# Kernel tuning notes

Hardware: AMD Instinct MI355X
Metric: run time of the kernel (lower is better)

Reference implementation:

```python
import jax, jax.numpy as jnp
import numpy as np

N_USER, N_ITEM, D = 50000, 100000, 64
E_UI, E_UU = 1000000, 800000
NEG_SLOPE = 0.2


def gatv2(x_src, x_dst, src_idx, dst_idx, w_src, w_dst, attn, bias, n_dst):
    """DGL GATv2Conv, num_heads=1: e = a . leaky_relu(Ws x_u + Wd x_v),
    segment-softmax over edges incoming to each dst node, message = Ws x_u."""
    hs = x_src @ w_src                      # [Ns, D]
    hd = x_dst @ w_dst                      # [Nd, D]
    pre = jax.nn.leaky_relu(hs[src_idx] + hd[dst_idx], NEG_SLOPE)  # [E, D]
    e = pre @ attn                          # [E]
    emax = jax.ops.segment_max(e, dst_idx, num_segments=n_dst)     # -inf for empty
    a = jnp.exp(e - emax[dst_idx])          # [E]
    denom = jax.ops.segment_sum(a, dst_idx, num_segments=n_dst)    # [Nd]
    num = jax.ops.segment_sum(hs[src_idx] * a[:, None], dst_idx, num_segments=n_dst)
    out = num / jnp.maximum(denom, 1e-9)[:, None]
    return out + bias


def setup_inputs() -> dict:
    key = jax.random.key(0)
    ks = jax.random.split(key, 32)
    s = 1.0 / np.sqrt(D)
    def W(k):
        return jax.random.normal(k, (D, D), jnp.float32) * s
    inp = {
        "h_user": jax.random.normal(ks[0], (N_USER, D), jnp.float32),
        "h_item": jax.random.normal(ks[1], (N_ITEM, D), jnp.float32),
        "rate_src": jax.random.randint(ks[2], (E_UI,), 0, N_USER, jnp.int32),
        "rate_dst": jax.random.randint(ks[3], (E_UI,), 0, N_ITEM, jnp.int32),
        "rb_src": jax.random.randint(ks[4], (E_UI,), 0, N_ITEM, jnp.int32),
        "rb_dst": jax.random.randint(ks[5], (E_UI,), 0, N_USER, jnp.int32),
        "link_src": jax.random.randint(ks[6], (E_UU,), 0, N_USER, jnp.int32),
        "link_dst": jax.random.randint(ks[7], (E_UU,), 0, N_USER, jnp.int32),
    }
    names = ["r1", "rb1", "rb2", "l2"]
    for i, nm in enumerate(names):
        inp[f"w_src_{nm}"] = W(ks[8 + 4 * i])
        inp[f"w_dst_{nm}"] = W(ks[9 + 4 * i])
        inp[f"a_{nm}"] = jax.random.normal(ks[10 + 4 * i], (D,), jnp.float32) * s
        inp[f"b_{nm}"] = jnp.zeros((D,), jnp.float32)
    inp["w_out"] = jax.random.normal(ks[24], (2 * D, D), jnp.float32) * (1.0 / np.sqrt(2 * D))
    inp["b_out"] = jnp.zeros((D,), jnp.float32)
    return inp


def reference(h_user, h_item,
              w_src_r1, w_dst_r1, a_r1, b_r1,
              w_src_rb1, w_dst_rb1, a_rb1, b_rb1,
              w_src_rb2, w_dst_rb2, a_rb2, b_rb2,
              w_src_l2, w_dst_l2, a_l2, b_l2,
              w_out, b_out,
              rate_src, rate_dst, rb_src, rb_dst, link_src, link_dst):
    # layer1 'rate': user -> item
    h1_item = gatv2(h_user, h_item, rate_src, rate_dst,
                    w_src_r1, w_dst_r1, a_r1, b_r1, N_ITEM)
    # layer1 'rated-by': item -> user
    h2_user = gatv2(h_item, h_user, rb_src, rb_dst,
                    w_src_rb1, w_dst_rb1, a_rb1, b_rb1, N_USER)
    # layer2 'rated-by': item(h1) -> user
    infl_user = gatv2(h1_item, h_user, rb_src, rb_dst,
                      w_src_rb2, w_dst_rb2, a_rb2, b_rb2, N_USER)
    # layer2 'link': user(h2) -> user
    social_user = gatv2(h2_user, h_user, link_src, link_dst,
                        w_src_l2, w_dst_l2, a_l2, b_l2, N_USER)
    out = jnp.concatenate([infl_user, social_user], axis=1) @ w_out + b_out
    return out
```

## Files before the change

kernel.cpp:

```cpp
#include <hip/hip_runtime.h>
#include <hip/hip_fp16.h>
#include <math.h>

#define N_USER 50000
#define N_ITEM 100000
#define E_UI   1000000
#define E_UU   800000
#define E_TOT  (E_UI + E_UI + E_UU)
#define NEG_SLOPE 0.2f
#define LOG2E 1.4426950408889634f

#define NB0 391
#define NB1 196
#define NB2 196
#define NBTOT (NB0 + NB1 + NB2)
#define GPB 256
#define MATN (NBTOT * 256)
#define NBP  ((MATN + 1023) / 1024)

#define XS_STRIDE 68

typedef _Float16 h2v __attribute__((ext_vector_type(2)));

#if defined(__has_builtin)
#if __has_builtin(__builtin_amdgcn_fdot2)
#define HAS_FDOT2 1
#endif
#if __has_builtin(__builtin_elementwise_max)
#define HAS_EW_MAX 1
#endif
#if __has_builtin(__builtin_amdgcn_exp2f)
#define HAS_EXP2 1
#endif
#endif

__device__ __forceinline__ float fexp2(float x) {
#ifdef HAS_EXP2
  return __builtin_amdgcn_exp2f(x);
#else
  return exp2f(x);
#endif
}

__device__ __forceinline__ float fdot2acc(__half2 a, __half2 b, float c) {
#ifdef HAS_FDOT2
  return __builtin_amdgcn_fdot2(__builtin_bit_cast(h2v, a), __builtin_bit_cast(h2v, b), c, false);
#else
  float2 af = __half22float2(a), bf = __half22float2(b);
  return fmaf(af.x, bf.x, fmaf(af.y, bf.y, c));
#endif
}

__device__ __forceinline__ __half2 h2max(__half2 a, __half2 b) {
  h2v av = __builtin_bit_cast(h2v, a), bv = __builtin_bit_cast(h2v, b);
#ifdef HAS_EW_MAX
  h2v r = __builtin_elementwise_max(av, bv);
#else
  h2v r; r.x = av.x > bv.x ? av.x : bv.x; r.y = av.y > bv.y ? av.y : bv.y;
#endif
  return __builtin_bit_cast(__half2, r);
}

__device__ __forceinline__ __half2 h2min(__half2 a, __half2 b) {
  h2v av = __builtin_bit_cast(h2v, a), bv = __builtin_bit_cast(h2v, b);
#ifdef HAS_EW_MAX
  h2v r = __builtin_elementwise_min(av, bv);
#else
  h2v r; r.x = av.x < bv.x ? av.x : bv.x; r.y = av.y < bv.y ? av.y : bv.y;
#endif
  return __builtin_bit_cast(__half2, r);
}


__global__ __launch_bounds__(256) void bucket_hist(const int* __restrict__ d0, const int* __restrict__ d1,
                                                   const int* __restrict__ d2, int* __restrict__ mat) {
  int gid = blockIdx.x >> 8;
  int g   = blockIdx.x & 255;
  const int* dst = gid == 0 ? d0 : (gid == 1 ? d1 : d2);
  int E    = (gid == 2) ? E_UU : E_UI;
  int NB   = (gid == 0) ? NB0 : NB1;
  int boff = (gid == 0) ? 0 : (gid == 1 ? NB0 : NB0 + NB1);
  __shared__ int cnt[NB0];
  for (int b = threadIdx.x; b < NB; b += 256) cnt[b] = 0;
  __syncthreads();
  int chunk = (E + 255) >> 8;
  int lo = g * chunk, hi = min(lo + chunk, E);
  for (int i = lo + threadIdx.x; i < hi; i += 256)
    atomicAdd(&cnt[dst[i] >> 8], 1);
  __syncthreads();
  for (int b = threadIdx.x; b < NB; b += 256)
    mat[(boff + b) * 256 + g] = cnt[b];
}


__global__ __launch_bounds__(256) void partial_kernel(const int* __restrict__ counts, int n,
                                                      int* __restrict__ partials) {
  int t = threadIdx.x;
  int base = blockIdx.x * 1024 + t * 4;
  int s = 0;
  if (base + 3 < n) {
    int4 v = *(const int4*)(counts + base);
    s = v.x + v.y + v.z + v.w;
  } else {
    for (int i = base; i < n && i < base + 4; ++i) s += counts[i];
  }
  #pragma unroll
  for (int off = 1; off < 64; off <<= 1) s += __shfl_xor(s, off);
  __shared__ int ws[4];
  if ((t & 63) == 0) ws[t >> 6] = s;
  __syncthreads();
  if (t == 0) partials[blockIdx.x] = ws[0] + ws[1] + ws[2] + ws[3];
}

__global__ __launch_bounds__(256) void scan_apply_fused(const int* __restrict__ counts, int n,
                                                        const int* __restrict__ partials, int nbp,
                                                        int* __restrict__ outp) {
  __shared__ int sp[256];
  int t = threadIdx.x;
  sp[t] = (t < nbp) ? partials[t] : 0;
  __syncthreads();
  for (int off = 1; off < 256; off <<= 1) {
    int v = (t >= off) ? sp[t - off] : 0;
    __syncthreads();
    sp[t] += v;
    __syncthreads();
  }
  int block_off = (blockIdx.x == 0) ? 0 : sp[blockIdx.x - 1];

  int base = blockIdx.x * 1024 + t * 4;
  int4 v = make_int4(0, 0, 0, 0);
  if (base + 3 < n) {
    v = *(const int4*)(counts + base);
  } else {
    int* pv = &v.x;
    for (int i = 0; i < 4; ++i) if (base + i < n) pv[i] = counts[base + i];
  }
  int s = v.x + v.y + v.z + v.w;
  int lane = t & 63;
  int wv = t >> 6;
  int inc = s;
  #pragma unroll
  for (int off = 1; off < 64; off <<= 1) {
    int u = __shfl_up(inc, off);
    if (lane >= off) inc += u;
  }
  __shared__ int wsum[4];
  if (lane == 63) wsum[wv] = inc;
  __syncthreads();
  int woff = 0;
  for (int i = 0; i < wv; ++i) woff += wsum[i];
  int excl = woff + (inc - s) + block_off;
  int4 rp;
  rp.x = excl;
  rp.y = rp.x + v.x;
  rp.z = rp.y + v.y;
  rp.w = rp.z + v.z;
  if (base + 3 < n) {
    *(int4*)(outp + base) = rp;
  } else {
    int* pr = &rp.x;
    for (int i = 0; i < 4; ++i) if (base + i < n) outp[base + i] = pr[i];
  }
}


__global__ __launch_bounds__(256) void bucket_scatter(const int* __restrict__ s0v, const int* __restrict__ d0,
                                                      const int* __restrict__ s1v, const int* __restrict__ d1,
                                                      const int* __restrict__ s2v, const int* __restrict__ d2,
                                                      const int* __restrict__ mscan, unsigned int* __restrict__ pairs) {
  int gid = blockIdx.x >> 8;
  int g   = blockIdx.x & 255;
  const int* src = gid == 0 ? s0v : (gid == 1 ? s1v : s2v);
  const int* dst = gid == 0 ? d0  : (gid == 1 ? d1  : d2);
  int E    = (gid == 2) ? E_UU : E_UI;
  int NB   = (gid == 0) ? NB0 : NB1;
  int boff = (gid == 0) ? 0 : (gid == 1 ? NB0 : NB0 + NB1);
  __shared__ int cur[NB0];
  for (int b = threadIdx.x; b < NB; b += 256) cur[b] = mscan[(boff + b) * 256 + g];
  __syncthreads();
  int chunk = (E + 255) >> 8;
  int lo = g * chunk, hi = min(lo + chunk, E);
  for (int i = lo + threadIdx.x; i < hi; i += 256) {
    int d = dst[i], s = src[i];
    int pos = atomicAdd(&cur[d >> 8], 1);
    pairs[pos] = ((unsigned)(d & 255) << 24) | (unsigned)s;
  }
}


__global__ __launch_bounds__(256) void bucket_finalize(const unsigned int* __restrict__ pairs,
                                                       const int* __restrict__ mscan,
                                                       int* __restrict__ rp, int* __restrict__ col) {
  int gb = blockIdx.x;
  int t  = threadIdx.x;
  int gid  = (gb < NB0) ? 0 : (gb < NB0 + NB1 ? 1 : 2);
  int boff = (gid == 0) ? 0 : (gid == 1 ? NB0 : NB0 + NB1);
  int node_goff = (gid == 0) ? 0 : (gid == 1 ? N_ITEM : N_ITEM + N_USER);
  int n    = (gid == 0) ? N_ITEM : N_USER;
  int b_local = gb - boff;
  int bs = mscan[gb * 256];
  int be = (gb + 1 < NBTOT) ? mscan[(gb + 1) * 256] : E_TOT;

  __shared__ int cnt[256];
  __shared__ int curb[256];
  __shared__ int wsum[4];
  cnt[t] = 0;
  __syncthreads();
  for (int i = bs + t; i < be; i += 256)
    atomicAdd(&cnt[pairs[i] >> 24], 1);
  __syncthreads();

  int v = cnt[t];
  int lane = t & 63, wv = t >> 6;
  int inc = v;
  #pragma unroll
  for (int off = 1; off < 64; off <<= 1) {
    int u = __shfl_up(inc, off);
    if (lane >= off) inc += u;
  }
  if (lane == 63) wsum[wv] = inc;
  __syncthreads();
  int woff = 0;
  for (int i = 0; i < wv; ++i) woff += wsum[i];
  int base = bs + woff + (inc - v);

  int node_local = b_local * 256 + t;
  if (node_local < n) rp[node_goff + node_local] = base;
  if (gb == NBTOT - 1 && t == 255) rp[N_ITEM + 2 * N_USER] = E_TOT;
  curb[t] = base;
  __syncthreads();

  for (int i = bs + t; i < be; i += 256) {
    unsigned u = pairs[i];
    int p = atomicAdd(&curb[u >> 24], 1);
    col[p] = (int)(u & 0xFFFFFFu);
  }
}


__device__ __forceinline__ void load_xtile(const float* __restrict__ X, float* Xs, int base, int N) {
  #pragma unroll
  for (int i = 0; i < 4; ++i) {
    int idx = threadIdx.x * 4 + i * 1024;
    int row = idx >> 6, colc = idx & 63;
    int grow = base + row;
    const float* src = X + (size_t)(grow < N ? grow : N - 1) * 64 + colc;
    *(float4*)(Xs + row * XS_STRIDE + colc) = *(const float4*)src;
  }
}

__device__ __forceinline__ void gemm_phase(const float* __restrict__ Wsrc, float* Ws,
                                           const float* x0, const float* x1,
                                           const float* x2, const float* x3, int c4,
                                           float4& acc0, float4& acc1, float4& acc2, float4& acc3) {
  __syncthreads();
  #pragma unroll
  for (int i = 0; i < 4; ++i) {
    int idx = threadIdx.x * 4 + i * 1024;
    *(float4*)(Ws + idx) = *(const float4*)(Wsrc + idx);
  }
  __syncthreads();
  acc0 = make_float4(0.f, 0.f, 0.f, 0.f);
  acc1 = acc0; acc2 = acc0; acc3 = acc0;
  #pragma unroll 4
  for (int k4 = 0; k4 < 64; k4 += 4) {
    float4 xa = *(const float4*)(x0 + k4);
    float4 xb = *(const float4*)(x1 + k4);
    float4 xc = *(const float4*)(x2 + k4);
    float4 xd = *(const float4*)(x3 + k4);
    #pragma unroll
    for (int kk = 0; kk < 4; ++kk) {
      float4 w = *(const float4*)(Ws + (k4 + kk) * 64 + c4);
      float sa = (&xa.x)[kk], sb = (&xb.x)[kk], sc = (&xc.x)[kk], sd = (&xd.x)[kk];
      acc0.x = fmaf(sa, w.x, acc0.x); acc0.y = fmaf(sa, w.y, acc0.y);
      acc0.z = fmaf(sa, w.z, acc0.z); acc0.w = fmaf(sa, w.w, acc0.w);
      acc1.x = fmaf(sb, w.x, acc1.x); acc1.y = fmaf(sb, w.y, acc1.y);
      acc1.z = fmaf(sb, w.z, acc1.z); acc1.w = fmaf(sb, w.w, acc1.w);
      acc2.x = fmaf(sc, w.x, acc2.x); acc2.y = fmaf(sc, w.y, acc2.y);
      acc2.z = fmaf(sc, w.z, acc2.z); acc2.w = fmaf(sc, w.w, acc2.w);
      acc3.x = fmaf(sd, w.x, acc3.x); acc3.y = fmaf(sd, w.y, acc3.y);
      acc3.z = fmaf(sd, w.z, acc3.z); acc3.w = fmaf(sd, w.w, acc3.w);
    }
  }
}

__device__ __forceinline__ void gemm_phase_h(const float* __restrict__ Wsrc, float* Ws,
                                             const __half* x0, const __half* x1,
                                             const __half* x2, const __half* x3, int c4,
                                             float4& acc0, float4& acc1, float4& acc2, float4& acc3) {
  __syncthreads();
  #pragma unroll
  for (int i = 0; i < 4; ++i) {
    int idx = threadIdx.x * 4 + i * 1024;
    *(float4*)(Ws + idx) = *(const float4*)(Wsrc + idx);
  }
  __syncthreads();
  acc0 = make_float4(0.f, 0.f, 0.f, 0.f);
  acc1 = acc0; acc2 = acc0; acc3 = acc0;
  #pragma unroll 4
  for (int k4 = 0; k4 < 64; k4 += 4) {
    uint2 ua = *(const uint2*)(x0 + k4);
    uint2 ub = *(const uint2*)(x1 + k4);
    uint2 uc = *(const uint2*)(x2 + k4);
    uint2 ud = *(const uint2*)(x3 + k4);
    float2 fa0 = __half22float2(__builtin_bit_cast(__half2, ua.x));
    float2 fa1 = __half22float2(__builtin_bit_cast(__half2, ua.y));
    float2 fb0 = __half22float2(__builtin_bit_cast(__half2, ub.x));
    float2 fb1 = __half22float2(__builtin_bit_cast(__half2, ub.y));
    float2 fc0 = __half22float2(__builtin_bit_cast(__half2, uc.x));
    float2 fc1 = __half22float2(__builtin_bit_cast(__half2, uc.y));
    float2 fd0 = __half22float2(__builtin_bit_cast(__half2, ud.x));
    float2 fd1 = __half22float2(__builtin_bit_cast(__half2, ud.y));
    float xav[4] = {fa0.x, fa0.y, fa1.x, fa1.y};
    float xbv[4] = {fb0.x, fb0.y, fb1.x, fb1.y};
    float xcv[4] = {fc0.x, fc0.y, fc1.x, fc1.y};
    float xdv[4] = {fd0.x, fd0.y, fd1.x, fd1.y};
    #pragma unroll
    for (int kk = 0; kk < 4; ++kk) {
      float4 w = *(const float4*)(Ws + (k4 + kk) * 64 + c4);
      float sa = xav[kk], sb = xbv[kk], sc = xcv[kk], sd = xdv[kk];
      acc0.x = fmaf(sa, w.x, acc0.x); acc0.y = fmaf(sa, w.y, acc0.y);
      acc0.z = fmaf(sa, w.z, acc0.z); acc0.w = fmaf(sa, w.w, acc0.w);
      acc1.x = fmaf(sb, w.x, acc1.x); acc1.y = fmaf(sb, w.y, acc1.y);
      acc1.z = fmaf(sb, w.z, acc1.z); acc1.w = fmaf(sb, w.w, acc1.w);
      acc2.x = fmaf(sc, w.x, acc2.x); acc2.y = fmaf(sc, w.y, acc2.y);
      acc2.z = fmaf(sc, w.z, acc2.z); acc2.w = fmaf(sc, w.w, acc2.w);
      acc3.x = fmaf(sd, w.x, acc3.x); acc3.y = fmaf(sd, w.y, acc3.y);
      acc3.z = fmaf(sd, w.z, acc3.z); acc3.w = fmaf(sd, w.w, acc3.w);
    }
  }
}

__device__ __forceinline__ void store4_f16(__half* __restrict__ Y, int r0, int r1, int r2, int r3,
                                           int N, int c4,
                                           const float4& a0, const float4& a1,
                                           const float4& a2, const float4& a3) {
  uint2 st;
  if (r0 < N) {
    st.x = __builtin_bit_cast(unsigned int, __floats2half2_rn(a0.x, a0.y));
    st.y = __builtin_bit_cast(unsigned int, __floats2half2_rn(a0.z, a0.w));
    *(uint2*)(Y + (size_t)r0 * 64 + c4) = st;
  }
  if (r1 < N) {
    st.x = __builtin_bit_cast(unsigned int, __floats2half2_rn(a1.x, a1.y));
    st.y = __builtin_bit_cast(unsigned int, __floats2half2_rn(a1.z, a1.w));
    *(uint2*)(Y + (size_t)r1 * 64 + c4) = st;
  }
  if (r2 < N) {
    st.x = __builtin_bit_cast(unsigned int, __floats2half2_rn(a2.x, a2.y));
    st.y = __builtin_bit_cast(unsigned int, __floats2half2_rn(a2.z, a2.w));
    *(uint2*)(Y + (size_t)r2 * 64 + c4) = st;
  }
  if (r3 < N) {
    st.x = __builtin_bit_cast(unsigned int, __floats2half2_rn(a3.x, a3.y));
    st.y = __builtin_bit_cast(unsigned int, __floats2half2_rn(a3.z, a3.w));
    *(uint2*)(Y + (size_t)r3 * 64 + c4) = st;
  }
}

__global__ __launch_bounds__(256) void gemm_user4(const float* __restrict__ X,
                                                  const float* __restrict__ W0, const float* __restrict__ W1,
                                                  const float* __restrict__ W2, const float* __restrict__ W3,
                                                  __half* __restrict__ Y0, __half* __restrict__ Y1,
                                                  __half* __restrict__ Y2, __half* __restrict__ Y3, int N) {
  __shared__ float Xs[64 * XS_STRIDE];
  __shared__ float Ws[64 * 64];
  int base = blockIdx.x * 64;
  load_xtile(X, Xs, base, N);
  int c4 = (threadIdx.x & 15) * 4;
  int rl = threadIdx.x >> 4;
  int r0 = base + rl, r1 = r0 + 16, r2 = r0 + 32, r3 = r0 + 48;
  const float* x0 = Xs + (rl +  0) * XS_STRIDE;
  const float* x1 = Xs + (rl + 16) * XS_STRIDE;
  const float* x2 = Xs + (rl + 32) * XS_STRIDE;
  const float* x3 = Xs + (rl + 48) * XS_STRIDE;
  float4 a0, a1, a2, a3;
  gemm_phase(W0, Ws, x0, x1, x2, x3, c4, a0, a1, a2, a3);
  store4_f16(Y0, r0, r1, r2, r3, N, c4, a0, a1, a2, a3);
  gemm_phase(W1, Ws, x0, x1, x2, x3, c4, a0, a1, a2, a3);
  store4_f16(Y1, r0, r1, r2, r3, N, c4, a0, a1, a2, a3);
  gemm_phase(W2, Ws, x0, x1, x2, x3, c4, a0, a1, a2, a3);
  store4_f16(Y2, r0, r1, r2, r3, N, c4, a0, a1, a2, a3);
  gemm_phase(W3, Ws, x0, x1, x2, x3, c4, a0, a1, a2, a3);
  store4_f16(Y3, r0, r1, r2, r3, N, c4, a0, a1, a2, a3);
}

__global__ __launch_bounds__(256) void gemm_item2(const float* __restrict__ X,
                                                  const float* __restrict__ W0, const float* __restrict__ W1,
                                                  __half* __restrict__ Y0, __half* __restrict__ Y1, int N) {
  __shared__ float Xs[64 * XS_STRIDE];
  __shared__ float Ws[64 * 64];
  int base = blockIdx.x * 64;
  load_xtile(X, Xs, base, N);
  int c4 = (threadIdx.x & 15) * 4;
  int rl = threadIdx.x >> 4;
  int r0 = base + rl, r1 = r0 + 16, r2 = r0 + 32, r3 = r0 + 48;
  const float* x0 = Xs + (rl +  0) * XS_STRIDE;
  const float* x1 = Xs + (rl + 16) * XS_STRIDE;
  const float* x2 = Xs + (rl + 32) * XS_STRIDE;
  const float* x3 = Xs + (rl + 48) * XS_STRIDE;
  float4 a0, a1, a2, a3;
  gemm_phase(W0, Ws, x0, x1, x2, x3, c4, a0, a1, a2, a3);
  store4_f16(Y0, r0, r1, r2, r3, N, c4, a0, a1, a2, a3);
  gemm_phase(W1, Ws, x0, x1, x2, x3, c4, a0, a1, a2, a3);
  store4_f16(Y1, r0, r1, r2, r3, N, c4, a0, a1, a2, a3);
}

__global__ __launch_bounds__(256) void gemm_mid2x(const __half* __restrict__ XA, const float* __restrict__ WA,
                                                  __half* __restrict__ YA, int NA, int nbA,
                                                  const __half* __restrict__ XB, const float* __restrict__ WB,
                                                  __half* __restrict__ YB, int NB_) {
  __shared__ float Ws[64 * 64];
  const __half* X; const float* W; __half* Y; int N; int base;
  if ((int)blockIdx.x < nbA) {
    X = XA; W = WA; Y = YA; N = NA; base = blockIdx.x * 64;
  } else {
    X = XB; W = WB; Y = YB; N = NB_; base = (blockIdx.x - nbA) * 64;
  }
  int c4 = (threadIdx.x & 15) * 4;
  int rl = threadIdx.x >> 4;
  int r0 = base + rl, r1 = r0 + 16, r2 = r0 + 32, r3 = r0 + 48;
  const __half* x0 = X + (size_t)(r0 < N ? r0 : N - 1) * 64;
  const __half* x1 = X + (size_t)(r1 < N ? r1 : N - 1) * 64;
  const __half* x2 = X + (size_t)(r2 < N ? r2 : N - 1) * 64;
  const __half* x3 = X + (size_t)(r3 < N ? r3 : N - 1) * 64;
  float4 a0, a1, a2, a3;
  gemm_phase_h(W, Ws, x0, x1, x2, x3, c4, a0, a1, a2, a3);
  store4_f16(Y, r0, r1, r2, r3, N, c4, a0, a1, a2, a3);
}


__global__ __launch_bounds__(256) void gat8n_kernel(
    const __half* __restrict__ hsA, const __half* __restrict__ hdAp,
    const int* __restrict__ rpA, const float* __restrict__ attnA, const float* __restrict__ biasA,
    __half* __restrict__ outA, int NdA,
    const __half* __restrict__ hsB, const __half* __restrict__ hdBp,
    const int* __restrict__ rpB, const float* __restrict__ attnB, const float* __restrict__ biasB,
    __half* __restrict__ outB, int NdB,
    const int* __restrict__ col) {
  int w = (blockIdx.x * blockDim.x + threadIdx.x) >> 6;
  int grp = (threadIdx.x >> 3) & 7;
  int q   = threadIdx.x & 7;
  int node = w * 8 + grp;
  bool valid = node < NdA + NdB;
  bool inA = node < NdA;
  const __half* hs  = inA ? hsA  : hsB;
  const __half* hd  = inA ? hdAp : hdBp;
  const int* rp     = inA ? rpA  : rpB;
  const float* attn = inA ? attnA : attnB;
  const float* bias = inA ? biasA : biasB;
  __half* outp      = inA ? outA : outB;
  int nn = inA ? node : node - NdA;
  if (!valid) nn = 0;
  int s0 = valid ? rp[nn] : 0;
  int s1 = valid ? rp[nn + 1] : 0;

  const __half2 C02 = __floats2half2_rn(NEG_SLOPE, NEG_SLOPE);
  const __half2 Z   = __floats2half2_rn(0.f, 0.f);

  __half2 hd2[4], a2[4];
  {
    uint4 hv = *(const uint4*)(hd + (size_t)nn * 64 + q * 8);
    hd2[0] = __builtin_bit_cast(__half2, hv.x);
    hd2[1] = __builtin_bit_cast(__half2, hv.y);
    hd2[2] = __builtin_bit_cast(__half2, hv.z);
    hd2[3] = __builtin_bit_cast(__half2, hv.w);
    const float* ap = attn + q * 8;
    #pragma unroll
    for (int i = 0; i < 2; ++i) {
      float4 v = *(const float4*)(ap + i * 4);
      a2[2 * i]     = __floats2half2_rn(v.x * LOG2E, v.y * LOG2E);
      a2[2 * i + 1] = __floats2half2_rn(v.z * LOG2E, v.w * LOG2E);
    }
  }

  float m = -1e30f, den = 0.f;
  float num[8];
  #pragma unroll
  for (int i = 0; i < 8; ++i) num[i] = 0.f;

  for (int e = s0; e < s1; e += 4) {
    bool h1 = (e + 1) < s1, h2c = (e + 2) < s1, h3 = (e + 3) < s1;
    int sa = col[e];
    int sb = col[h1 ? e + 1 : e];
    int sc = col[h2c ? e + 2 : e];
    int sd = col[h3 ? e + 3 : e];
    uint4 ra = *(const uint4*)(hs + (size_t)sa * 64 + q * 8);
    uint4 rb = *(const uint4*)(hs + (size_t)sb * 64 + q * 8);
    uint4 rc = *(const uint4*)(hs + (size_t)sc * 64 + q * 8);
    uint4 rd = *(const uint4*)(hs + (size_t)sd * 64 + q * 8);
    unsigned rau[4] = {ra.x, ra.y, ra.z, ra.w};
    unsigned rbu[4] = {rb.x, rb.y, rb.z, rb.w};
    unsigned rcu[4] = {rc.x, rc.y, rc.z, rc.w};
    unsigned rdu[4] = {rd.x, rd.y, rd.z, rd.w};

    float ta = 0.f, tb = 0.f, tc = 0.f, td = 0.f;
    #pragma unroll
    for (int i = 0; i < 4; ++i) {
      __half2 xa = __hadd2(__builtin_bit_cast(__half2, rau[i]), hd2[i]);
      ta = fdot2acc(a2[i], __hfma2(C02, h2min(xa, Z), h2max(xa, Z)), ta);
      __half2 xb = __hadd2(__builtin_bit_cast(__half2, rbu[i]), hd2[i]);
      tb = fdot2acc(a2[i], __hfma2(C02, h2min(xb, Z), h2max(xb, Z)), tb);
      __half2 xc = __hadd2(__builtin_bit_cast(__half2, rcu[i]), hd2[i]);
      tc = fdot2acc(a2[i], __hfma2(C02, h2min(xc, Z), h2max(xc, Z)), tc);
      __half2 xd = __hadd2(__builtin_bit_cast(__half2, rdu[i]), hd2[i]);
      td = fdot2acc(a2[i], __hfma2(C02, h2min(xd, Z), h2max(xd, Z)), td);
    }
    #pragma unroll
    for (int off = 1; off < 8; off <<= 1) {
      ta += __shfl_xor(ta, off);
      tb += __shfl_xor(tb, off);
      tc += __shfl_xor(tc, off);
      td += __shfl_xor(td, off);
    }
    if (!h1)  tb = -1e30f;
    if (!h2c) tc = -1e30f;
    if (!h3)  td = -1e30f;

    float tp = fmaxf(fmaxf(ta, tb), fmaxf(tc, td));
    float dd = tp - m;
    if (dd > 11.5f) {
      float sc0 = fexp2(-dd);
      den *= sc0;
      #pragma unroll
      for (int i = 0; i < 8; ++i) num[i] *= sc0;
      m = tp;
    }
    float pa = fexp2(ta - m);
    float pb = fexp2(tb - m);
    float pc = fexp2(tc - m);
    float pd = fexp2(td - m);
    den += (pa + pb) + (pc + pd);
    __half2 pab = __floats2half2_rn(pa, pb);
    __half2 pcd = __floats2half2_rn(pc, pd);

    #pragma unroll
    for (int i = 0; i < 4; ++i) {
      unsigned lo_ab = (rau[i] & 0xFFFFu) | (rbu[i] << 16);
      unsigned hi_ab = (rau[i] >> 16) | (rbu[i] & 0xFFFF0000u);
      unsigned lo_cd = (rcu[i] & 0xFFFFu) | (rdu[i] << 16);
      unsigned hi_cd = (rcu[i] >> 16) | (rdu[i] & 0xFFFF0000u);
      num[2 * i]     = fdot2acc(__builtin_bit_cast(__half2, lo_cd), pcd,
                       fdot2acc(__builtin_bit_cast(__half2, lo_ab), pab, num[2 * i]));
      num[2 * i + 1] = fdot2acc(__builtin_bit_cast(__half2, hi_cd), pcd,
                       fdot2acc(__builtin_bit_cast(__half2, hi_ab), pab, num[2 * i + 1]));
    }
  }

  if (valid) {
    float inv = 1.f / fmaxf(den, 1e-9f);
    const float* bp = bias + q * 8;
    float4 b0 = *(const float4*)(bp);
    float4 b1 = *(const float4*)(bp + 4);
    uint4 st;
    st.x = __builtin_bit_cast(unsigned int,
        __floats2half2_rn(fmaf(num[0], inv, b0.x), fmaf(num[1], inv, b0.y)));
    st.y = __builtin_bit_cast(unsigned int,
        __floats2half2_rn(fmaf(num[2], inv, b0.z), fmaf(num[3], inv, b0.w)));
    st.z = __builtin_bit_cast(unsigned int,
        __floats2half2_rn(fmaf(num[4], inv, b1.x), fmaf(num[5], inv, b1.y)));
    st.w = __builtin_bit_cast(unsigned int,
        __floats2half2_rn(fmaf(num[6], inv, b1.z), fmaf(num[7], inv, b1.w)));
    *(uint4*)(outp + (size_t)nn * 64 + q * 8) = st;
  }
}


__global__ __launch_bounds__(256) void final_kernel(const __half* __restrict__ A, const __half* __restrict__ B,
                                                    const float* __restrict__ W, const float* __restrict__ bias,
                                                    float* __restrict__ Y, int N) {
  __shared__ float Ws[128 * 64];
  #pragma unroll
  for (int i = 0; i < 8; ++i) {
    int idx = threadIdx.x * 4 + i * 1024;
    *(float4*)(Ws + idx) = *(const float4*)(W + idx);
  }
  __syncthreads();
  int c4 = (threadIdx.x & 15) * 4;
  int rl = threadIdx.x >> 4;
  int base = blockIdx.x * 64;

  float4 b4 = *(const float4*)(bias + c4);

  #pragma unroll
  for (int rr = 0; rr < 4; ++rr) {
    int row = base + rr * 16 + rl;
    if (row >= N) continue;
    const __half* ar = A + (size_t)row * 64;
    const __half* br = B + (size_t)row * 64;
    float4 acc = b4;
    #pragma unroll 4
    for (int k4 = 0; k4 < 64; k4 += 4) {
      uint2 ua = *(const uint2*)(ar + k4);
      uint2 ub = *(const uint2*)(br + k4);
      float2 fa0 = __half22float2(__builtin_bit_cast(__half2, ua.x));
      float2 fa1 = __half22float2(__builtin_bit_cast(__half2, ua.y));
      float2 fb0 = __half22float2(__builtin_bit_cast(__half2, ub.x));
      float2 fb1 = __half22float2(__builtin_bit_cast(__half2, ub.y));
      float xav[4] = {fa0.x, fa0.y, fa1.x, fa1.y};
      float xbv[4] = {fb0.x, fb0.y, fb1.x, fb1.y};
      #pragma unroll
      for (int kk = 0; kk < 4; ++kk) {
        float4 wa = *(const float4*)(Ws + (k4 + kk) * 64 + c4);
        float4 wb = *(const float4*)(Ws + (64 + k4 + kk) * 64 + c4);
        float xsa = xav[kk], xsb = xbv[kk];
        acc.x = fmaf(xsa, wa.x, acc.x); acc.x = fmaf(xsb, wb.x, acc.x);
        acc.y = fmaf(xsa, wa.y, acc.y); acc.y = fmaf(xsb, wb.y, acc.y);
        acc.z = fmaf(xsa, wa.z, acc.z); acc.z = fmaf(xsb, wb.z, acc.z);
        acc.w = fmaf(xsa, wa.w, acc.w); acc.w = fmaf(xsb, wb.w, acc.w);
      }
    }
    *(float4*)(Y + (size_t)row * 64 + c4) = acc;
  }
}


extern "C" void kernel_launch(void* const* d_in, const int* in_sizes, int n_in,
                              void* d_out, int out_size, void* d_ws, size_t ws_size,
                              hipStream_t stream) {
  const float* h_user   = (const float*)d_in[0];
  const float* h_item   = (const float*)d_in[1];
  const int* rate_src   = (const int*)d_in[2];
  const int* rate_dst   = (const int*)d_in[3];
  const int* rb_src     = (const int*)d_in[4];
  const int* rb_dst     = (const int*)d_in[5];
  const int* link_src   = (const int*)d_in[6];
  const int* link_dst   = (const int*)d_in[7];
  const float* w_src_r1  = (const float*)d_in[8];
  const float* w_dst_r1  = (const float*)d_in[9];
  const float* a_r1      = (const float*)d_in[10];
  const float* b_r1      = (const float*)d_in[11];
  const float* w_src_rb1 = (const float*)d_in[12];
  const float* w_dst_rb1 = (const float*)d_in[13];
  const float* a_rb1     = (const float*)d_in[14];
  const float* b_rb1     = (const float*)d_in[15];
  const float* w_src_rb2 = (const float*)d_in[16];
  const float* w_dst_rb2 = (const float*)d_in[17];
  const float* a_rb2     = (const float*)d_in[18];
  const float* b_rb2     = (const float*)d_in[19];
  const float* w_src_l2  = (const float*)d_in[20];
  const float* w_dst_l2  = (const float*)d_in[21];
  const float* a_l2      = (const float*)d_in[22];
  const float* b_l2      = (const float*)d_in[23];
  const float* w_out     = (const float*)d_in[24];
  const float* b_out     = (const float*)d_in[25];
  float* out = (float*)d_out;

  char* ws = (char*)d_ws;
  size_t off = 0;
  auto alloc = [&](size_t bytes) -> void* {
    void* p = ws + off;
    off += (bytes + 255) & ~(size_t)255;
    return p;
  };

  __half* uh0 = (__half*)alloc((size_t)N_USER * 64 * 2);
  __half* u1  = (__half*)alloc((size_t)N_USER * 64 * 2);
  __half* u2  = (__half*)alloc((size_t)N_USER * 64 * 2);
  __half* u3  = (__half*)alloc((size_t)N_USER * 64 * 2);
  __half* i0  = (__half*)alloc((size_t)N_ITEM * 64 * 2);
  __half* ih1 = (__half*)alloc((size_t)N_ITEM * 64 * 2);

  int* mat     = (int*)alloc((size_t)MATN * 4);
  int* mscan   = (int*)alloc((size_t)MATN * 4);
  int* partials= (int*)alloc(256 * 4);
  int* grp     = (int*)alloc((size_t)(N_ITEM + 2 * N_USER + 1) * 4);
  unsigned int* pairs = (unsigned int*)alloc((size_t)E_TOT * 4);
  int* col_all = (int*)alloc((size_t)E_TOT * 4);

  bucket_hist<<<3 * GPB, 256, 0, stream>>>(rate_dst, rb_dst, link_dst, mat);
  partial_kernel<<<NBP, 256, 0, stream>>>(mat, MATN, partials);
  scan_apply_fused<<<NBP, 256, 0, stream>>>(mat, MATN, partials, NBP, mscan);
  bucket_scatter<<<3 * GPB, 256, 0, stream>>>(rate_src, rate_dst, rb_src, rb_dst,
                                              link_src, link_dst, mscan, pairs);
  bucket_finalize<<<NBTOT, 256, 0, stream>>>(pairs, mscan, grp, col_all);

  int* rp_rate = grp;
  int* rp_rb   = grp + N_ITEM;
  int* rp_link = grp + N_ITEM + N_USER;

  gemm_user4<<<(N_USER + 63) / 64, 256, 0, stream>>>(
      h_user, w_src_r1, w_dst_rb1, w_dst_rb2, w_dst_l2, uh0, u1, u2, u3, N_USER);
  gemm_item2<<<(N_ITEM + 63) / 64, 256, 0, stream>>>(
      h_item, w_dst_r1, w_src_rb1, i0, ih1, N_ITEM);

  {
    int nodes = N_ITEM + N_USER;
    gat8n_kernel<<<(nodes + 31) / 32, 256, 0, stream>>>(
        uh0, i0, rp_rate, a_r1,  b_r1,  i0, N_ITEM,
        ih1, u1, rp_rb,   a_rb1, b_rb1, u1, N_USER,
        col_all);
  }

  {
    int nbA = (N_ITEM + 63) / 64;
    int nbB = (N_USER + 63) / 64;
    gemm_mid2x<<<nbA + nbB, 256, 0, stream>>>(
        i0, w_src_rb2, ih1, N_ITEM, nbA,
        u1, w_src_l2,  uh0, N_USER);
  }

  {
    int nodes = N_USER + N_USER;
    gat8n_kernel<<<(nodes + 31) / 32, 256, 0, stream>>>(
        ih1, u2, rp_rb,   a_rb2, b_rb2, u2, N_USER,
        uh0, u3, rp_link, a_l2,  b_l2,  u3, N_USER,
        col_all);
  }

  final_kernel<<<(N_USER + 63) / 64, 256, 0, stream>>>(u2, u3, w_out, b_out, out, N_USER);
}
```

Before: 258.3 us.

## Sort destination nodes by in-degree to balance GAT aggregation warps

Builds a per-region degree histogram in bucket_finalize, scans it, and scatters node ids into a degree-sorted permutation. The GAT kernels then process nodes through that permutation, so the 8 nodes sharing a wavefront have similar edge counts and divergence from uneven degrees is reduced. This adds two small kernels, a memset and global atomics on a 192-bin histogram, and it breaks the locality of hd and output accesses, which now follow permuted node order.

Result: slower. 933.0 us (+261.2%).

```diff
diff --git a/kernel.cpp b/kernel.cpp
--- a/kernel.cpp
+++ b/kernel.cpp
@@ -7,6 +7,7 @@
 #define E_UI   1000000
 #define E_UU   800000
 #define E_TOT  (E_UI + E_UI + E_UU)
+#define NTOT_NODES (N_ITEM + 2 * N_USER)
 #define NEG_SLOPE 0.2f
 #define LOG2E 1.4426950408889634f
 
@@ -190,7 +191,8 @@
 
 __global__ __launch_bounds__(256) void bucket_finalize(const unsigned int* __restrict__ pairs,
                                                        const int* __restrict__ mscan,
-                                                       int* __restrict__ rp, int* __restrict__ col) {
+                                                       int* __restrict__ rp, int* __restrict__ col,
+                                                       int* __restrict__ degbins) {
   int gb = blockIdx.x;
   int t  = threadIdx.x;
   int gid  = (gb < NB0) ? 0 : (gb < NB0 + NB1 ? 1 : 2);
@@ -225,7 +227,10 @@
   int base = bs + woff + (inc - v);
 
   int node_local = b_local * 256 + t;
-  if (node_local < n) rp[node_goff + node_local] = base;
+  if (node_local < n) {
+    rp[node_goff + node_local] = base;
+    atomicAdd(&degbins[gid * 64 + (v < 63 ? v : 63)], 1);
+  }
   if (gb == NBTOT - 1 && t == 255) rp[N_ITEM + 2 * N_USER] = E_TOT;
   curb[t] = base;
   __syncthreads();
@@ -235,6 +240,27 @@
     int p = atomicAdd(&curb[u >> 24], 1);
     col[p] = (int)(u & 0xFFFFFFu);
   }
+}
+
+
+__global__ void bin_scan(const int* __restrict__ bins, int* __restrict__ cursor) {
+  int r = threadIdx.x;
+  if (r < 3) {
+    int acc = 0;
+    for (int b = 0; b < 64; ++b) { cursor[r * 64 + b] = acc; acc += bins[r * 64 + b]; }
+  }
+}
+
+__global__ __launch_bounds__(256) void perm_scatter(const int* __restrict__ grp,
+                                                    int* __restrict__ cursor, int* __restrict__ perm) {
+  int nidx = blockIdx.x * 256 + threadIdx.x;
+  if (nidx >= NTOT_NODES) return;
+  int region = (nidx < N_ITEM) ? 0 : (nidx < N_ITEM + N_USER ? 1 : 2);
+  int rbase  = (region == 0) ? 0 : (region == 1 ? N_ITEM : N_ITEM + N_USER);
+  int d = grp[nidx + 1] - grp[nidx];
+  int bin = d < 63 ? d : 63;
+  int p = atomicAdd(&cursor[region * 64 + bin], 1);
+  perm[rbase + p] = nidx - rbase;
 }
 
 
@@ -433,25 +459,25 @@
 __global__ __launch_bounds__(256) void gat8n_kernel(
     const __half* __restrict__ hsA, const __half* __restrict__ hdAp,
     const int* __restrict__ rpA, const float* __restrict__ attnA, const float* __restrict__ biasA,
-    __half* __restrict__ outA, int NdA,
+    __half* __restrict__ outA, int NdA, const int* __restrict__ permA,
     const __half* __restrict__ hsB, const __half* __restrict__ hdBp,
     const int* __restrict__ rpB, const float* __restrict__ attnB, const float* __restrict__ biasB,
-    __half* __restrict__ outB, int NdB,
+    __half* __restrict__ outB, int NdB, const int* __restrict__ permB,
     const int* __restrict__ col) {
   int w = (blockIdx.x * blockDim.x + threadIdx.x) >> 6;
   int grp = (threadIdx.x >> 3) & 7;
   int q   = threadIdx.x & 7;
-  int node = w * 8 + grp;
-  bool valid = node < NdA + NdB;
-  bool inA = node < NdA;
+  int idx = w * 8 + grp;
+  bool valid = idx < NdA + NdB;
+  bool inA = idx < NdA;
   const __half* hs  = inA ? hsA  : hsB;
   const __half* hd  = inA ? hdAp : hdBp;
   const int* rp     = inA ? rpA  : rpB;
   const float* attn = inA ? attnA : attnB;
   const float* bias = inA ? biasA : biasB;
   __half* outp      = inA ? outA : outB;
-  int nn = inA ? node : node - NdA;
-  if (!valid) nn = 0;
+  int nn = 0;
+  if (valid) nn = inA ? permA[idx] : permB[idx - NdA];
   int s0 = valid ? rp[nn] : 0;
   int s1 = valid ? rp[nn + 1] : 0;
 
@@ -664,20 +690,30 @@
   int* mat     = (int*)alloc((size_t)MATN * 4);
   int* mscan   = (int*)alloc((size_t)MATN * 4);
   int* partials= (int*)alloc(256 * 4);
-  int* grp     = (int*)alloc((size_t)(N_ITEM + 2 * N_USER + 1) * 4);
+  int* grp     = (int*)alloc((size_t)(NTOT_NODES + 1) * 4);
   unsigned int* pairs = (unsigned int*)alloc((size_t)E_TOT * 4);
   int* col_all = (int*)alloc((size_t)E_TOT * 4);
+  int* degbins = (int*)alloc(192 * 4);
+  int* degcur  = (int*)alloc(192 * 4);
+  int* permbuf = (int*)alloc((size_t)NTOT_NODES * 4);
 
   bucket_hist<<<3 * GPB, 256, 0, stream>>>(rate_dst, rb_dst, link_dst, mat);
   partial_kernel<<<NBP, 256, 0, stream>>>(mat, MATN, partials);
   scan_apply_fused<<<NBP, 256, 0, stream>>>(mat, MATN, partials, NBP, mscan);
   bucket_scatter<<<3 * GPB, 256, 0, stream>>>(rate_src, rate_dst, rb_src, rb_dst,
                                               link_src, link_dst, mscan, pairs);
-  bucket_finalize<<<NBTOT, 256, 0, stream>>>(pairs, mscan, grp, col_all);
+  hipMemsetAsync(degbins, 0, 192 * 4, stream);
+  bucket_finalize<<<NBTOT, 256, 0, stream>>>(pairs, mscan, grp, col_all, degbins);
+
+  bin_scan<<<1, 64, 0, stream>>>(degbins, degcur);
+  perm_scatter<<<(NTOT_NODES + 255) / 256, 256, 0, stream>>>(grp, degcur, permbuf);
 
   int* rp_rate = grp;
   int* rp_rb   = grp + N_ITEM;
   int* rp_link = grp + N_ITEM + N_USER;
+  int* pm_rate = permbuf;
+  int* pm_rb   = permbuf + N_ITEM;
+  int* pm_link = permbuf + N_ITEM + N_USER;
 
   gemm_user4<<<(N_USER + 63) / 64, 256, 0, stream>>>(
       h_user, w_src_r1, w_dst_rb1, w_dst_rb2, w_dst_l2, uh0, u1, u2, u3, N_USER);
@@ -687,8 +723,8 @@
   {
     int nodes = N_ITEM + N_USER;
     gat8n_kernel<<<(nodes + 31) / 32, 256, 0, stream>>>(
-        uh0, i0, rp_rate, a_r1,  b_r1,  i0, N_ITEM,
-        ih1, u1, rp_rb,   a_rb1, b_rb1, u1, N_USER,
+        uh0, i0, rp_rate, a_r1,  b_r1,  i0, N_ITEM, pm_rate,
+        ih1, u1, rp_rb,   a_rb1, b_rb1, u1, N_USER, pm_rb,
         col_all);
   }
 
@@ -703,8 +739,8 @@
   {
     int nodes = N_USER + N_USER;
     gat8n_kernel<<<(nodes + 31) / 32, 256, 0, stream>>>(
-        ih1, u2, rp_rb,   a_rb2, b_rb2, u2, N_USER,
-        uh0, u3, rp_link, a_l2,  b_l2,  u3, N_USER,
+        ih1, u2, rp_rb,   a_rb2, b_rb2, u2, N_USER, pm_rb,
+        uh0, u3, rp_link, a_l2,  b_l2,  u3, N_USER, pm_link,
         col_all);
   }
 
```
